# Kernel tuning notes

Measured on AMD Instinct MI355X. Metric: run time of the kernel, lower is better.

The kernel has to match this reference:

```python
import jax, jax.numpy as jnp
import numpy as np

N = 100000   # nodes
E = 1600000  # edges
IN = 128
HID = 64
HEADS = 2
OUT = 16
G = 100      # graphs in batch
NEG_SLOPE = 0.2


def setup_inputs() -> dict:
    key = jax.random.key(0)
    ks = jax.random.split(key, 14)
    s = 0.05
    return {
        "x": jax.random.normal(ks[0], (N, IN), jnp.float32),
        "edge_index": jax.random.randint(ks[1], (2, E), 0, N, dtype=jnp.int32),
        "batch": jnp.sort(jax.random.randint(ks[2], (N,), 0, G, dtype=jnp.int32)),
        "W1": jax.random.normal(ks[3], (IN, HEADS * HID), jnp.float32) * s,
        "att_src1": jax.random.normal(ks[4], (HEADS, HID), jnp.float32) * s,
        "att_dst1": jax.random.normal(ks[5], (HEADS, HID), jnp.float32) * s,
        "b1": jax.random.normal(ks[6], (HEADS * HID,), jnp.float32) * s,
        "W2": jax.random.normal(ks[7], (HEADS * HID, HID), jnp.float32) * s,
        "att_src2": jax.random.normal(ks[8], (1, HID), jnp.float32) * s,
        "att_dst2": jax.random.normal(ks[9], (1, HID), jnp.float32) * s,
        "b2": jax.random.normal(ks[10], (HID,), jnp.float32) * s,
        "Wl": jax.random.normal(ks[11], (HID, OUT), jnp.float32) * s,
        "bl": jax.random.normal(ks[12], (OUT,), jnp.float32) * s,
    }


def gat_conv(x, src, dst, W, a_src, a_dst, b, heads, out_c):
    """PyG GATConv: transform, per-edge attention, segment softmax over dst, scatter-add."""
    n = x.shape[0]
    h = (x @ W).reshape(n, heads, out_c)              # [N, H, C]
    alpha_src = (h * a_src).sum(-1)                   # [N, H]
    alpha_dst = (h * a_dst).sum(-1)                   # [N, H]
    e = jax.nn.leaky_relu(alpha_src[src] + alpha_dst[dst], NEG_SLOPE)  # [Etot, H]
    m = jax.ops.segment_max(e, dst, num_segments=n)   # stable softmax per dst
    ex = jnp.exp(e - m[dst])
    den = jax.ops.segment_sum(ex, dst, num_segments=n)
    alpha = ex / den[dst]                             # [Etot, H]
    msg = h[src] * alpha[..., None]                   # [Etot, H, C]
    out = jax.ops.segment_sum(msg, dst, num_segments=n)
    return out.reshape(n, heads * out_c) + b


def reference(x, edge_index, batch, W1, att_src1, att_dst1, b1,
              W2, att_src2, att_dst2, b2, Wl, bl):
    n = x.shape[0]
    loop = jnp.arange(n, dtype=edge_index.dtype)      # PyG add_self_loops default
    src = jnp.concatenate([edge_index[0], loop])
    dst = jnp.concatenate([edge_index[1], loop])
    h = gat_conv(x, src, dst, W1, att_src1, att_dst1, b1, HEADS, HID)
    h = jax.nn.relu(h)
    h = gat_conv(h, src, dst, W2, att_src2, att_dst2, b2, 1, HID)
    sums = jax.ops.segment_sum(h, batch, num_segments=G)
    cnt = jax.ops.segment_sum(jnp.ones((n,), h.dtype), batch, num_segments=G)
    pooled = sums / jnp.maximum(cnt, 1.0)[:, None]    # global_mean_pool
    return pooled @ Wl + bl
```

## Files before the change

kernel.cpp:

```cpp
#include <hip/hip_runtime.h>
#include <math.h>

#define GRAPHS 100
#define HIDC 64
#define OUTC 16
#define SLOPE 0.2f
#define BSHIFT 8
#define MAXNB 512
#define BKT_CAP 10240

typedef unsigned short ushort_t;
typedef short bf16x8 __attribute__((ext_vector_type(8)));
typedef float f32x4 __attribute__((ext_vector_type(4)));
typedef ushort_t u16x8 __attribute__((ext_vector_type(8)));
typedef ushort_t u16x4 __attribute__((ext_vector_type(4)));

__device__ __forceinline__ float lrelu(float v) { return v > 0.f ? v : SLOPE * v; }
__device__ __forceinline__ void atomAddG(float* p, float v) { unsafeAtomicAdd(p, v); }
__device__ __forceinline__ float bf2f(ushort_t u) {
    unsigned int x = ((unsigned int)u) << 16;
    return __builtin_bit_cast(float, x);
}
__device__ __forceinline__ ushort_t f2bf(float f) {
    unsigned int u = __builtin_bit_cast(unsigned int, f);
    u += 0x7FFFu + ((u >> 16) & 1u);
    return (ushort_t)(u >> 16);
}
__device__ __forceinline__ unsigned int pack2(float lo, float hi) {
    return (unsigned int)f2bf(lo) | ((unsigned int)f2bf(hi) << 16);
}

template <bool A_IS_BF16, int ASTRIDE>
__global__ __launch_bounds__(256) void mfma_gemm_alpha(const void* __restrict__ Av,
                                                       const float* __restrict__ W,
                                                       ushort_t* __restrict__ Cbf,
                                                       const float* __restrict__ att_src,
                                                       const float* __restrict__ att_dst,
                                                       float* __restrict__ asrc,
                                                       float* __restrict__ adst,
                                                       int M, int K, int N) {
    __shared__ ushort_t As[64 * 40];
    __shared__ ushort_t Bs[64 * 40];
    __shared__ float ps[2][64], pd[2][64];
    const int tid = threadIdx.x;
    const int row0 = blockIdx.x * 64;
    const int col0 = blockIdx.y * 64;
    const int lane = tid & 63;
    const int wv = tid >> 6;
    const int wr = (wv >> 1) * 32, wc = (wv & 1) * 32;
    const int l15 = lane & 15, l4 = lane >> 4;

    const int srow = tid >> 2;
    const int skoff = (tid & 3) * 8;
    const int bc = tid & 63, bk = (tid >> 6) * 8;

    f32x4 acc[2][2] = {};

    for (int k0 = 0; k0 < K; k0 += 32) {
        {
            int gr = row0 + srow;
            uint4 v = {0u, 0u, 0u, 0u};
            if (gr < M) {
                if (A_IS_BF16) {
                    const ushort_t* Ab = (const ushort_t*)Av;
                    v = *(const uint4*)(Ab + (size_t)gr * K + k0 + skoff);
                } else {
                    const float* Af = (const float*)Av;
                    const float4 a0 = *(const float4*)(Af + (size_t)gr * K + k0 + skoff);
                    const float4 a1 = *(const float4*)(Af + (size_t)gr * K + k0 + skoff + 4);
                    v.x = pack2(a0.x, a0.y);
                    v.y = pack2(a0.z, a0.w);
                    v.z = pack2(a1.x, a1.y);
                    v.w = pack2(a1.z, a1.w);
                }
            }
            *(uint4*)&As[srow * 40 + skoff] = v;
        }
        {
#pragma unroll
            for (int j = 0; j < 8; ++j) {
                float w = W[(size_t)(k0 + bk + j) * N + col0 + bc];
                Bs[bc * 40 + bk + j] = f2bf(w);
            }
        }
        __syncthreads();
        bf16x8 af[2], bfr[2];
#pragma unroll
        for (int mi = 0; mi < 2; ++mi)
            af[mi] = *(const bf16x8*)&As[(wr + mi * 16 + l15) * 40 + l4 * 8];
#pragma unroll
        for (int ni = 0; ni < 2; ++ni)
            bfr[ni] = *(const bf16x8*)&Bs[(wc + ni * 16 + l15) * 40 + l4 * 8];
#pragma unroll
        for (int mi = 0; mi < 2; ++mi)
#pragma unroll
            for (int ni = 0; ni < 2; ++ni)
                acc[mi][ni] = __builtin_amdgcn_mfma_f32_16x16x32_bf16(af[mi], bfr[ni],
                                                                     acc[mi][ni], 0, 0, 0);
        __syncthreads();
    }
#pragma unroll
    for (int mi = 0; mi < 2; ++mi)
#pragma unroll
        for (int ni = 0; ni < 2; ++ni)
#pragma unroll
            for (int r = 0; r < 4; ++r) {
                int row = row0 + wr + mi * 16 + l4 * 4 + r;
                int colg = col0 + wc + ni * 16 + l15;
                if (row < M) Cbf[(size_t)row * N + colg] = f2bf(acc[mi][ni][r]);
            }
    float as_c[2], ad_c[2];
#pragma unroll
    for (int ni = 0; ni < 2; ++ni) {
        int cidx = col0 + wc + ni * 16 + l15;
        as_c[ni] = att_src[cidx];
        ad_c[ni] = att_dst[cidx];
    }
#pragma unroll
    for (int mi = 0; mi < 2; ++mi)
#pragma unroll
        for (int r = 0; r < 4; ++r) {
            float s = acc[mi][0][r] * as_c[0] + acc[mi][1][r] * as_c[1];
            float d = acc[mi][0][r] * ad_c[0] + acc[mi][1][r] * ad_c[1];
#pragma unroll
            for (int off = 1; off < 16; off <<= 1) {
                s += __shfl_xor(s, off);
                d += __shfl_xor(d, off);
            }
            if (l15 == 0) {
                int rl = wr + mi * 16 + l4 * 4 + r;
                ps[wc >> 5][rl] = s;
                pd[wc >> 5][rl] = d;
            }
        }
    __syncthreads();
    if (tid < 64) {
        int row = row0 + tid;
        if (row < M) {
            asrc[ASTRIDE * row + blockIdx.y] = ps[0][tid] + ps[1][tid];
            adst[ASTRIDE * row + blockIdx.y] = pd[0][tid] + pd[1][tid];
        }
    }
}

__global__ __launch_bounds__(256) void bucket_hist(const int* __restrict__ ei, int E,
                                                   int* __restrict__ bcnt, int NB) {
    __shared__ int h[MAXNB];
    for (int t = threadIdx.x; t < NB; t += 256) h[t] = 0;
    __syncthreads();
    int chunk = (E + gridDim.x - 1) / gridDim.x;
    int e0 = blockIdx.x * chunk;
    int e1 = e0 + chunk < E ? e0 + chunk : E;
    for (int e = e0 + threadIdx.x; e < e1; e += 256)
        atomicAdd(&h[ei[E + e] >> BSHIFT], 1);
    __syncthreads();
    for (int t = threadIdx.x; t < NB; t += 256)
        if (h[t]) atomicAdd(&bcnt[t], h[t]);
}

__global__ __launch_bounds__(512) void bucket_scan(const int* __restrict__ bcnt,
                                                   int* __restrict__ bbase,
                                                   int* __restrict__ bcursor,
                                                   int* __restrict__ rowptr,
                                                   int NB, int n, int E) {
    __shared__ int sh[512];
    int t = threadIdx.x;
    int v = (t < NB) ? bcnt[t] : 0;
    sh[t] = v;
    __syncthreads();
#pragma unroll
    for (int off = 1; off < 512; off <<= 1) {
        int val = (t >= off) ? sh[t - off] : 0;
        __syncthreads();
        sh[t] += val;
        __syncthreads();
    }
    if (t < NB) {
        int base = sh[t] - v;
        bbase[t] = base;
        bcursor[t] = base;
    }
    if (t == 0) {
        bbase[NB] = E;
        rowptr[n] = E;
    }
}

__global__ __launch_bounds__(256) void bucket_scatter(const int* __restrict__ ei, int E,
                                                      int* __restrict__ bcursor,
                                                      unsigned int* __restrict__ ebuf, int NB) {
    __shared__ int h[MAXNB];
    __shared__ int lbase[MAXNB];
    for (int t = threadIdx.x; t < NB; t += 256) h[t] = 0;
    __syncthreads();
    int chunk = (E + gridDim.x - 1) / gridDim.x;
    int e0 = blockIdx.x * chunk;
    int e1 = e0 + chunk < E ? e0 + chunk : E;
    for (int e = e0 + threadIdx.x; e < e1; e += 256)
        atomicAdd(&h[ei[E + e] >> BSHIFT], 1);
    __syncthreads();
    for (int t = threadIdx.x; t < NB; t += 256) {
        int c = h[t];
        lbase[t] = c ? atomicAdd(&bcursor[t], c) : 0;
        h[t] = 0;
    }
    __syncthreads();
    for (int e = e0 + threadIdx.x; e < e1; e += 256) {
        int d = ei[E + e];
        int s = ei[e];
        int b = d >> BSHIFT;
        int off = atomicAdd(&h[b], 1);
        ebuf[lbase[b] + off] = (unsigned)s | ((unsigned)(d & ((1 << BSHIFT) - 1)) << 24);
    }
}

__global__ __launch_bounds__(256) void bucket_build(const unsigned int* __restrict__ ebuf,
                                                    const int* __restrict__ bbase,
                                                    int* __restrict__ rowptr,
                                                    int* __restrict__ col, int n) {
    __shared__ int hist[256];
    __shared__ int curs[256];
    __shared__ int sh[256];
    __shared__ int lsrc[BKT_CAP];
    int b = blockIdx.x;
    int e0 = bbase[b], e1 = bbase[b + 1];
    int cnt = e1 - e0;
    int t = threadIdx.x;
    hist[t] = 0;
    __syncthreads();
    for (int k = t; k < cnt; k += 256) atomicAdd(&hist[ebuf[e0 + k] >> 24], 1);
    __syncthreads();
    int v = hist[t];
    sh[t] = v;
    __syncthreads();
#pragma unroll
    for (int off = 1; off < 256; off <<= 1) {
        int val = (t >= off) ? sh[t - off] : 0;
        __syncthreads();
        sh[t] += val;
        __syncthreads();
    }
    int ex = sh[t] - v;
    curs[t] = ex;
    int node = (b << BSHIFT) + t;
    if (node < n) rowptr[node] = e0 + ex;
    __syncthreads();
    for (int k = t; k < cnt; k += 256) {
        unsigned pk = ebuf[e0 + k];
        int ld = pk >> 24;
        int off = atomicAdd(&curs[ld], 1);
        if (off < BKT_CAP) lsrc[off] = (int)(pk & 0xFFFFFFu);
    }
    __syncthreads();
    int lim = cnt < BKT_CAP ? cnt : BKT_CAP;
    for (int k = t; k < lim; k += 256) col[e0 + k] = lsrc[k];
}

__global__ __launch_bounds__(256) void gat_agg1(const int* __restrict__ rowptr,
                                                const int* __restrict__ col,
                                                const ushort_t* __restrict__ h,
                                                const float* __restrict__ asrc,
                                                const float* __restrict__ adst,
                                                const float* __restrict__ b1,
                                                ushort_t* __restrict__ outb, int n) {
    int i = (blockIdx.x * blockDim.x + threadIdx.x) >> 6;
    if (i >= n) return;
    int lane = threadIdx.x & 63;
    int grp = lane >> 4, c = lane & 15;
    int head = c >> 3;
    float ad = adst[2 * i + head];
    const u16x8* h8 = (const u16x8*)h;
    float acc[8] = {};
    float den = 0.f;
    if (grp == 0) {
        float w = __expf(lrelu(asrc[2 * i + head] + ad));
        u16x8 hv = h8[(size_t)i * 16 + c];
#pragma unroll
        for (int j = 0; j < 8; ++j) acc[j] = bf2f(hv[j]) * w;
        den = w;
    }
    int e0 = rowptr[i], end = rowptr[i + 1];
    for (int e = e0; e < end; e += 16) {
        float wv[4];
        u16x8 hv[4];
#pragma unroll
        for (int q = 0; q < 4; ++q) {
            int idx = e + 4 * q + grp;
            bool vld = idx < end;
            int s = col[vld ? idx : e0];
            float as = asrc[2 * s + head];
            hv[q] = h8[(size_t)s * 16 + c];
            wv[q] = vld ? __expf(lrelu(as + ad)) : 0.f;
        }
#pragma unroll
        for (int q = 0; q < 4; ++q) {
#pragma unroll
            for (int j = 0; j < 8; ++j) acc[j] = fmaf(bf2f(hv[q][j]), wv[q], acc[j]);
            den += wv[q];
        }
    }
#pragma unroll
    for (int j = 0; j < 8; ++j) {
        acc[j] += __shfl_xor(acc[j], 16);
        acc[j] += __shfl_xor(acc[j], 32);
    }
    den += __shfl_xor(den, 16);
    den += __shfl_xor(den, 32);
    if (grp == 0) {
        float inv = 1.f / den;
        u16x8 ov;
#pragma unroll
        for (int j = 0; j < 8; ++j) {
            float r = fmaf(acc[j], inv, b1[8 * c + j]);
            r = r > 0.f ? r : 0.f;
            ov[j] = f2bf(r);
        }
        *((u16x8*)outb + (size_t)i * 16 + c) = ov;
    }
}

__global__ __launch_bounds__(256) void gat_agg2(const int* __restrict__ rowptr,
                                                const int* __restrict__ col,
                                                const ushort_t* __restrict__ h,
                                                const float* __restrict__ asrc,
                                                const float* __restrict__ adst,
                                                ushort_t* __restrict__ outb, int n) {
    int i = (blockIdx.x * blockDim.x + threadIdx.x) >> 6;
    if (i >= n) return;
    int lane = threadIdx.x & 63;
    int grp = lane >> 4, c = lane & 15;
    float ad = adst[i];
    const u16x4* h4 = (const u16x4*)h;
    float acc[4] = {};
    float den = 0.f;
    if (grp == 0) {
        float w = __expf(lrelu(asrc[i] + ad));
        u16x4 hv = h4[(size_t)i * 16 + c];
#pragma unroll
        for (int j = 0; j < 4; ++j) acc[j] = bf2f(hv[j]) * w;
        den = w;
    }
    int e0 = rowptr[i], end = rowptr[i + 1];
    for (int e = e0; e < end; e += 16) {
        float wv[4];
        u16x4 hv[4];
#pragma unroll
        for (int q = 0; q < 4; ++q) {
            int idx = e + 4 * q + grp;
            bool vld = idx < end;
            int s = col[vld ? idx : e0];
            float as = asrc[s];
            hv[q] = h4[(size_t)s * 16 + c];
            wv[q] = vld ? __expf(lrelu(as + ad)) : 0.f;
        }
#pragma unroll
        for (int q = 0; q < 4; ++q) {
#pragma unroll
            for (int j = 0; j < 4; ++j) acc[j] = fmaf(bf2f(hv[q][j]), wv[q], acc[j]);
            den += wv[q];
        }
    }
#pragma unroll
    for (int j = 0; j < 4; ++j) {
        acc[j] += __shfl_xor(acc[j], 16);
        acc[j] += __shfl_xor(acc[j], 32);
    }
    den += __shfl_xor(den, 16);
    den += __shfl_xor(den, 32);
    if (grp == 0) {
        float inv = 1.f / den;
        u16x4 ov = {f2bf(acc[0] * inv), f2bf(acc[1] * inv), f2bf(acc[2] * inv),
                    f2bf(acc[3] * inv)};
        *((u16x4*)outb + (size_t)i * 16 + c) = ov;
    }
}

#define NPB 256
__global__ __launch_bounds__(256) void pool_kernel(const ushort_t* __restrict__ h,
                                                   const int* __restrict__ batch,
                                                   float* __restrict__ sums,
                                                   float* __restrict__ cnt, int n) {
    __shared__ float ls[GRAPHS * HIDC];
    __shared__ float lc[GRAPHS];
    int base = blockIdx.x * NPB;
    for (int t = threadIdx.x; t < GRAPHS * HIDC; t += blockDim.x) ls[t] = 0.f;
    for (int t = threadIdx.x; t < GRAPHS; t += blockDim.x) lc[t] = 0.f;
    __syncthreads();
    int wave = threadIdx.x >> 6, lane = threadIdx.x & 63;
    int end = base + NPB < n ? base + NPB : n;
    for (int i = base + wave; i < end; i += 4) {
        int g = batch[i];
        unsafeAtomicAdd(&ls[g * HIDC + lane], bf2f(h[(size_t)i * HIDC + lane]));
        if (lane == 0) unsafeAtomicAdd(&lc[g], 1.f);
    }
    __syncthreads();
    int gmin = batch[base];
    int gmax = batch[end - 1];
    int ng = gmax - gmin + 1;
    for (int t = threadIdx.x; t < ng * HIDC; t += blockDim.x) {
        int g = gmin + t / HIDC, c = t % HIDC;
        atomAddG(&sums[g * HIDC + c], ls[g * HIDC + c]);
    }
    for (int g = gmin + (int)threadIdx.x; g <= gmax; g += blockDim.x)
        atomAddG(&cnt[g], lc[g]);
}

__global__ void final_kernel(const float* __restrict__ sums, const float* __restrict__ cnt,
                             const float* __restrict__ b2, const float* __restrict__ Wl,
                             const float* __restrict__ bl, float* __restrict__ out) {
    int t = blockIdx.x * blockDim.x + threadIdx.x;
    if (t < GRAPHS * OUTC) {
        int g = t / OUTC, o = t % OUTC;
        float c = cnt[g];
        c = c > 1.f ? c : 1.f;
        float inv = 1.f / c;
        float acc = bl[o];
        for (int k = 0; k < HIDC; ++k)
            acc += (sums[g * HIDC + k] * inv + b2[k]) * Wl[k * OUTC + o];
        out[t] = acc;
    }
}

extern "C" void kernel_launch(void* const* d_in, const int* in_sizes, int n_in, void* d_out,
                              int out_size, void* d_ws, size_t ws_size, hipStream_t stream) {
    const float* x = (const float*)d_in[0];
    const int* ei = (const int*)d_in[1];
    const int* batch = (const int*)d_in[2];
    const float* W1 = (const float*)d_in[3];
    const float* att_src1 = (const float*)d_in[4];
    const float* att_dst1 = (const float*)d_in[5];
    const float* b1 = (const float*)d_in[6];
    const float* W2 = (const float*)d_in[7];
    const float* att_src2 = (const float*)d_in[8];
    const float* att_dst2 = (const float*)d_in[9];
    const float* b2 = (const float*)d_in[10];
    const float* Wl = (const float*)d_in[11];
    const float* bl = (const float*)d_in[12];
    float* out = (float*)d_out;

    const int n = in_sizes[2];
    const int E = in_sizes[1] / 2;

    char* p = (char*)d_ws;
    auto alloc = [&](size_t bytes) {
        char* r = p;
        p += (bytes + 255) & ~(size_t)255;
        return r;
    };
    ushort_t* h1 = (ushort_t*)alloc((size_t)n * 128 * 2);
    ushort_t* hrelu = (ushort_t*)alloc((size_t)n * 128 * 2);
    ushort_t* h2 = (ushort_t*)alloc((size_t)n * 64 * 2);
    ushort_t* conv2 = (ushort_t*)alloc((size_t)n * 64 * 2);
    float* asrc1 = (float*)alloc((size_t)n * 2 * 4);
    float* adst1 = (float*)alloc((size_t)n * 2 * 4);
    float* asrc2 = (float*)alloc((size_t)n * 4);
    float* adst2 = (float*)alloc((size_t)n * 4);
    float* sums = (float*)alloc(GRAPHS * HIDC * 4);
    float* cnt = (float*)alloc(GRAPHS * 4);
    int* bcnt = (int*)alloc(MAXNB * 4);
    int* bbase = (int*)alloc((MAXNB + 1) * 4);
    int* bcursor = (int*)alloc(MAXNB * 4);
    int* rowptr = (int*)alloc(((size_t)n + 1) * 4);
    unsigned int* ebuf = (unsigned int*)alloc((size_t)E * 4);
    int* col = (int*)alloc((size_t)E * 4);

    const int NB = (n + 255) >> BSHIFT;
    const int gblk = (n + 63) / 64;

    hipMemsetAsync(bcnt, 0, NB * sizeof(int), stream);
    bucket_hist<<<512, 256, 0, stream>>>(ei, E, bcnt, NB);
    bucket_scan<<<1, 512, 0, stream>>>(bcnt, bbase, bcursor, rowptr, NB, n, E);
    bucket_scatter<<<512, 256, 0, stream>>>(ei, E, bcursor, ebuf, NB);
    bucket_build<<<NB, 256, 0, stream>>>(ebuf, bbase, rowptr, col, n);

    mfma_gemm_alpha<false, 2><<<dim3(gblk, 2), 256, 0, stream>>>(
        x, W1, h1, att_src1, att_dst1, asrc1, adst1, n, 128, 128);
    gat_agg1<<<(n + 3) / 4, 256, 0, stream>>>(rowptr, col, h1, asrc1, adst1, b1, hrelu, n);

    mfma_gemm_alpha<true, 1><<<dim3(gblk, 1), 256, 0, stream>>>(
        hrelu, W2, h2, att_src2, att_dst2, asrc2, adst2, n, 128, 64);
    gat_agg2<<<(n + 3) / 4, 256, 0, stream>>>(rowptr, col, h2, asrc2, adst2, conv2, n);

    hipMemsetAsync(sums, 0, (GRAPHS * HIDC + GRAPHS) * sizeof(float), stream);
    pool_kernel<<<(n + NPB - 1) / NPB, 256, 0, stream>>>(conv2, batch, sums, cnt, n);
    final_kernel<<<(GRAPHS * OUTC + 255) / 256, 256, 0, stream>>>(sums, cnt, b2, Wl, bl, out);
}
```

Baseline: 363.2 us.

## Fuse edge scatter with layer-1 GEMM and pack bf16 FMAs in aggregation

Merges the bucket scatter kernel and the first-layer GEMM+attention kernel into one launch, with blocks split by index, so the two independent stages run concurrently and one launch is saved. The zeroing of the pooling buffers moves into the scan kernel, which removes a memset. The aggregation kernels now decode bf16 pairs straight from 32-bit words and use 2-wide vector FMAs (packed-math candidates), with 32-bit byte-offset addressing in place of 64-bit index math. The fused kernel's shared-memory footprint is the union of both stages, which may lower occupancy, and the unsigned offsets assume node offsets stay under 4 GB.

```diff
diff --git a/kernel.cpp b/kernel.cpp
--- a/kernel.cpp
+++ b/kernel.cpp
@@ -8,10 +8,12 @@
 #define BSHIFT 8
 #define MAXNB 512
 #define BKT_CAP 10240
+#define SCAT_BLOCKS 512
 
 typedef unsigned short ushort_t;
 typedef short bf16x8 __attribute__((ext_vector_type(8)));
 typedef float f32x4 __attribute__((ext_vector_type(4)));
+typedef float f32x2 __attribute__((ext_vector_type(2)));
 typedef ushort_t u16x8 __attribute__((ext_vector_type(8)));
 typedef ushort_t u16x4 __attribute__((ext_vector_type(4)));
 
@@ -29,27 +31,26 @@
 __device__ __forceinline__ unsigned int pack2(float lo, float hi) {
     return (unsigned int)f2bf(lo) | ((unsigned int)f2bf(hi) << 16);
 }
+__device__ __forceinline__ void mac2(unsigned int u, float w, f32x2& a) {
+    f32x2 hv;
+    hv.x = __builtin_bit_cast(float, u << 16);
+    hv.y = __builtin_bit_cast(float, u & 0xFFFF0000u);
+    f32x2 w2 = {w, w};
+    a = __builtin_elementwise_fma(hv, w2, a);
+}
 
 template <bool A_IS_BF16, int ASTRIDE>
-__global__ __launch_bounds__(256) void mfma_gemm_alpha(const void* __restrict__ Av,
-                                                       const float* __restrict__ W,
-                                                       ushort_t* __restrict__ Cbf,
-                                                       const float* __restrict__ att_src,
-                                                       const float* __restrict__ att_dst,
-                                                       float* __restrict__ asrc,
-                                                       float* __restrict__ adst,
-                                                       int M, int K, int N) {
-    __shared__ ushort_t As[64 * 40];
-    __shared__ ushort_t Bs[64 * 40];
-    __shared__ float ps[2][64], pd[2][64];
+__device__ __forceinline__ void gemm_alpha_body(
+    const void* __restrict__ Av, const float* __restrict__ W, ushort_t* __restrict__ Cbf,
+    const float* __restrict__ att_src, const float* __restrict__ att_dst,
+    float* __restrict__ asrc, float* __restrict__ adst, int M, int K, int N,
+    int row0, int head, ushort_t* As, ushort_t* Bs, float (*ps)[64], float (*pd)[64]) {
     const int tid = threadIdx.x;
-    const int row0 = blockIdx.x * 64;
-    const int col0 = blockIdx.y * 64;
+    const int col0 = head * 64;
     const int lane = tid & 63;
     const int wv = tid >> 6;
     const int wr = (wv >> 1) * 32, wc = (wv & 1) * 32;
     const int l15 = lane & 15, l4 = lane >> 4;
-
     const int srow = tid >> 2;
     const int skoff = (tid & 3) * 8;
     const int bc = tid & 63, bk = (tid >> 6) * 8;
@@ -137,10 +138,26 @@
     if (tid < 64) {
         int row = row0 + tid;
         if (row < M) {
-            asrc[ASTRIDE * row + blockIdx.y] = ps[0][tid] + ps[1][tid];
-            adst[ASTRIDE * row + blockIdx.y] = pd[0][tid] + pd[1][tid];
-        }
-    }
+            asrc[ASTRIDE * row + head] = ps[0][tid] + ps[1][tid];
+            adst[ASTRIDE * row + head] = pd[0][tid] + pd[1][tid];
+        }
+    }
+}
+
+template <bool A_IS_BF16, int ASTRIDE>
+__global__ __launch_bounds__(256) void mfma_gemm_alpha(const void* __restrict__ Av,
+                                                       const float* __restrict__ W,
+                                                       ushort_t* __restrict__ Cbf,
+                                                       const float* __restrict__ att_src,
+                                                       const float* __restrict__ att_dst,
+                                                       float* __restrict__ asrc,
+                                                       float* __restrict__ adst,
+                                                       int M, int K, int N) {
+    __shared__ ushort_t As[64 * 40];
+    __shared__ ushort_t Bs[64 * 40];
+    __shared__ float ps[2][64], pd[2][64];
+    gemm_alpha_body<A_IS_BF16, ASTRIDE>(Av, W, Cbf, att_src, att_dst, asrc, adst, M, K, N,
+                                        blockIdx.x * 64, blockIdx.y, As, Bs, ps, pd);
 }
 
 __global__ __launch_bounds__(256) void bucket_hist(const int* __restrict__ ei, int E,
@@ -162,6 +179,8 @@
                                                    int* __restrict__ bbase,
                                                    int* __restrict__ bcursor,
                                                    int* __restrict__ rowptr,
+                                                   float* __restrict__ sums,
+                                                   float* __restrict__ cnt,
                                                    int NB, int n, int E) {
     __shared__ int sh[512];
     int t = threadIdx.x;
@@ -184,33 +203,49 @@
         bbase[NB] = E;
         rowptr[n] = E;
     }
-}
-
-__global__ __launch_bounds__(256) void bucket_scatter(const int* __restrict__ ei, int E,
-                                                      int* __restrict__ bcursor,
-                                                      unsigned int* __restrict__ ebuf, int NB) {
-    __shared__ int h[MAXNB];
+    for (int k = t; k < GRAPHS * HIDC; k += 512) sums[k] = 0.f;
+    for (int k = t; k < GRAPHS; k += 512) cnt[k] = 0.f;
+}
+
+__global__ __launch_bounds__(256) void scatter_gemm1(
+    const int* __restrict__ ei, int E, int* __restrict__ bcursor,
+    unsigned int* __restrict__ ebuf, int NB,
+    const float* __restrict__ x, const float* __restrict__ W, ushort_t* __restrict__ h1,
+    const float* __restrict__ att_src, const float* __restrict__ att_dst,
+    float* __restrict__ asrc, float* __restrict__ adst, int M, int gblk) {
+    __shared__ ushort_t As[64 * 40];
+    __shared__ ushort_t Bs[64 * 40];
+    __shared__ float ps[2][64], pd[2][64];
+    __shared__ int hh[MAXNB];
     __shared__ int lbase[MAXNB];
-    for (int t = threadIdx.x; t < NB; t += 256) h[t] = 0;
-    __syncthreads();
-    int chunk = (E + gridDim.x - 1) / gridDim.x;
-    int e0 = blockIdx.x * chunk;
-    int e1 = e0 + chunk < E ? e0 + chunk : E;
-    for (int e = e0 + threadIdx.x; e < e1; e += 256)
-        atomicAdd(&h[ei[E + e] >> BSHIFT], 1);
-    __syncthreads();
-    for (int t = threadIdx.x; t < NB; t += 256) {
-        int c = h[t];
-        lbase[t] = c ? atomicAdd(&bcursor[t], c) : 0;
-        h[t] = 0;
-    }
-    __syncthreads();
-    for (int e = e0 + threadIdx.x; e < e1; e += 256) {
-        int d = ei[E + e];
-        int s = ei[e];
-        int b = d >> BSHIFT;
-        int off = atomicAdd(&h[b], 1);
-        ebuf[lbase[b] + off] = (unsigned)s | ((unsigned)(d & ((1 << BSHIFT) - 1)) << 24);
+    if ((int)blockIdx.x < SCAT_BLOCKS) {
+        for (int t = threadIdx.x; t < NB; t += 256) hh[t] = 0;
+        __syncthreads();
+        int chunk = (E + SCAT_BLOCKS - 1) / SCAT_BLOCKS;
+        int e0 = blockIdx.x * chunk;
+        int e1 = e0 + chunk < E ? e0 + chunk : E;
+        for (int e = e0 + threadIdx.x; e < e1; e += 256)
+            atomicAdd(&hh[ei[E + e] >> BSHIFT], 1);
+        __syncthreads();
+        for (int t = threadIdx.x; t < NB; t += 256) {
+            int c = hh[t];
+            lbase[t] = c ? atomicAdd(&bcursor[t], c) : 0;
+            hh[t] = 0;
+        }
+        __syncthreads();
+        for (int e = e0 + threadIdx.x; e < e1; e += 256) {
+            int d = ei[E + e];
+            int s = ei[e];
+            int b = d >> BSHIFT;
+            int off = atomicAdd(&hh[b], 1);
+            ebuf[lbase[b] + off] = (unsigned)s | ((unsigned)(d & ((1 << BSHIFT) - 1)) << 24);
+        }
+    } else {
+        int bid = blockIdx.x - SCAT_BLOCKS;
+        int head = bid / gblk;
+        int row0 = (bid - head * gblk) * 64;
+        gemm_alpha_body<false, 2>(x, W, h1, att_src, att_dst, asrc, adst, M, 128, 128,
+                                  row0, head, As, Bs, ps, pd);
     }
 }
 
@@ -268,41 +303,50 @@
     int lane = threadIdx.x & 63;
     int grp = lane >> 4, c = lane & 15;
     int head = c >> 3;
+    const char* hb = (const char*)h;
+    const char* ab = (const char*)asrc;
     float ad = adst[2 * i + head];
-    const u16x8* h8 = (const u16x8*)h;
-    float acc[8] = {};
+    f32x2 acc2[4] = {};
     float den = 0.f;
+    unsigned coff = (unsigned)c << 4;
     if (grp == 0) {
         float w = __expf(lrelu(asrc[2 * i + head] + ad));
-        u16x8 hv = h8[(size_t)i * 16 + c];
-#pragma unroll
-        for (int j = 0; j < 8; ++j) acc[j] = bf2f(hv[j]) * w;
+        uint4 hq = *(const uint4*)(hb + (((unsigned)i << 8) + coff));
+        mac2(hq.x, w, acc2[0]);
+        mac2(hq.y, w, acc2[1]);
+        mac2(hq.z, w, acc2[2]);
+        mac2(hq.w, w, acc2[3]);
         den = w;
     }
     int e0 = rowptr[i], end = rowptr[i + 1];
+    unsigned aoff = ((unsigned)head << 2);
     for (int e = e0; e < end; e += 16) {
         float wv[4];
-        u16x8 hv[4];
+        uint4 hq[4];
 #pragma unroll
         for (int q = 0; q < 4; ++q) {
             int idx = e + 4 * q + grp;
             bool vld = idx < end;
             int s = col[vld ? idx : e0];
-            float as = asrc[2 * s + head];
-            hv[q] = h8[(size_t)s * 16 + c];
+            float as = *(const float*)(ab + (((unsigned)s << 3) + aoff));
+            hq[q] = *(const uint4*)(hb + (((unsigned)s << 8) + coff));
             wv[q] = vld ? __expf(lrelu(as + ad)) : 0.f;
         }
 #pragma unroll
         for (int q = 0; q < 4; ++q) {
-#pragma unroll
-            for (int j = 0; j < 8; ++j) acc[j] = fmaf(bf2f(hv[q][j]), wv[q], acc[j]);
+            mac2(hq[q].x, wv[q], acc2[0]);
+            mac2(hq[q].y, wv[q], acc2[1]);
+            mac2(hq[q].z, wv[q], acc2[2]);
+            mac2(hq[q].w, wv[q], acc2[3]);
             den += wv[q];
         }
     }
 #pragma unroll
-    for (int j = 0; j < 8; ++j) {
-        acc[j] += __shfl_xor(acc[j], 16);
-        acc[j] += __shfl_xor(acc[j], 32);
+    for (int k = 0; k < 4; ++k) {
+        acc2[k].x += __shfl_xor(acc2[k].x, 16);
+        acc2[k].x += __shfl_xor(acc2[k].x, 32);
+        acc2[k].y += __shfl_xor(acc2[k].y, 16);
+        acc2[k].y += __shfl_xor(acc2[k].y, 32);
     }
     den += __shfl_xor(den, 16);
     den += __shfl_xor(den, 32);
@@ -310,10 +354,13 @@
         float inv = 1.f / den;
         u16x8 ov;
 #pragma unroll
-        for (int j = 0; j < 8; ++j) {
-            float r = fmaf(acc[j], inv, b1[8 * c + j]);
-            r = r > 0.f ? r : 0.f;
-            ov[j] = f2bf(r);
+        for (int k = 0; k < 4; ++k) {
+            float r0 = fmaf(acc2[k].x, inv, b1[8 * c + 2 * k]);
+            float r1 = fmaf(acc2[k].y, inv, b1[8 * c + 2 * k + 1]);
+            r0 = r0 > 0.f ? r0 : 0.f;
+            r1 = r1 > 0.f ? r1 : 0.f;
+            ov[2 * k] = f2bf(r0);
+            ov[2 * k + 1] = f2bf(r1);
         }
         *((u16x8*)outb + (size_t)i * 16 + c) = ov;
     }
@@ -329,48 +376,52 @@
     if (i >= n) return;
     int lane = threadIdx.x & 63;
     int grp = lane >> 4, c = lane & 15;
+    const char* hb = (const char*)h;
+    const char* ab = (const char*)asrc;
     float ad = adst[i];
-    const u16x4* h4 = (const u16x4*)h;
-    float acc[4] = {};
+    f32x2 acc2[2] = {};
     float den = 0.f;
+    unsigned coff = (unsigned)c << 3;
     if (grp == 0) {
         float w = __expf(lrelu(asrc[i] + ad));
-        u16x4 hv = h4[(size_t)i * 16 + c];
-#pragma unroll
-        for (int j = 0; j < 4; ++j) acc[j] = bf2f(hv[j]) * w;
+        uint2 hq = *(const uint2*)(hb + (((unsigned)i << 7) + coff));
+        mac2(hq.x, w, acc2[0]);
+        mac2(hq.y, w, acc2[1]);
         den = w;
     }
     int e0 = rowptr[i], end = rowptr[i + 1];
     for (int e = e0; e < end; e += 16) {
         float wv[4];
-        u16x4 hv[4];
+        uint2 hq[4];
 #pragma unroll
         for (int q = 0; q < 4; ++q) {
             int idx = e + 4 * q + grp;
             bool vld = idx < end;
             int s = col[vld ? idx : e0];
-            float as = asrc[s];
-            hv[q] = h4[(size_t)s * 16 + c];
+            float as = *(const float*)(ab + ((unsigned)s << 2));
+            hq[q] = *(const uint2*)(hb + (((unsigned)s << 7) + coff));
             wv[q] = vld ? __expf(lrelu(as + ad)) : 0.f;
         }
 #pragma unroll
         for (int q = 0; q < 4; ++q) {
-#pragma unroll
-            for (int j = 0; j < 4; ++j) acc[j] = fmaf(bf2f(hv[q][j]), wv[q], acc[j]);
+            mac2(hq[q].x, wv[q], acc2[0]);
+            mac2(hq[q].y, wv[q], acc2[1]);
             den += wv[q];
         }
     }
 #pragma unroll
-    for (int j = 0; j < 4; ++j) {
-        acc[j] += __shfl_xor(acc[j], 16);
-        acc[j] += __shfl_xor(acc[j], 32);
+    for (int k = 0; k < 2; ++k) {
+        acc2[k].x += __shfl_xor(acc2[k].x, 16);
+        acc2[k].x += __shfl_xor(acc2[k].x, 32);
+        acc2[k].y += __shfl_xor(acc2[k].y, 16);
+        acc2[k].y += __shfl_xor(acc2[k].y, 32);
     }
     den += __shfl_xor(den, 16);
     den += __shfl_xor(den, 32);
     if (grp == 0) {
         float inv = 1.f / den;
-        u16x4 ov = {f2bf(acc[0] * inv), f2bf(acc[1] * inv), f2bf(acc[2] * inv),
-                    f2bf(acc[3] * inv)};
+        u16x4 ov = {f2bf(acc2[0].x * inv), f2bf(acc2[0].y * inv), f2bf(acc2[1].x * inv),
+                    f2bf(acc2[1].y * inv)};
         *((u16x4*)outb + (size_t)i * 16 + c) = ov;
     }
 }
@@ -468,20 +519,18 @@
     const int gblk = (n + 63) / 64;
 
     hipMemsetAsync(bcnt, 0, NB * sizeof(int), stream);
-    bucket_hist<<<512, 256, 0, stream>>>(ei, E, bcnt, NB);
-    bucket_scan<<<1, 512, 0, stream>>>(bcnt, bbase, bcursor, rowptr, NB, n, E);
-    bucket_scatter<<<512, 256, 0, stream>>>(ei, E, bcursor, ebuf, NB);
+    bucket_hist<<<SCAT_BLOCKS, 256, 0, stream>>>(ei, E, bcnt, NB);
+    bucket_scan<<<1, 512, 0, stream>>>(bcnt, bbase, bcursor, rowptr, sums, cnt, NB, n, E);
+    scatter_gemm1<<<SCAT_BLOCKS + 2 * gblk, 256, 0, stream>>>(
+        ei, E, bcursor, ebuf, NB, x, W1, h1, att_src1, att_dst1, asrc1, adst1, n, gblk);
     bucket_build<<<NB, 256, 0, stream>>>(ebuf, bbase, rowptr, col, n);
 
-    mfma_gemm_alpha<false, 2><<<dim3(gblk, 2), 256, 0, stream>>>(
-        x, W1, h1, att_src1, att_dst1, asrc1, adst1, n, 128, 128);
     gat_agg1<<<(n + 3) / 4, 256, 0, stream>>>(rowptr, col, h1, asrc1, adst1, b1, hrelu, n);
 
     mfma_gemm_alpha<true, 1><<<dim3(gblk, 1), 256, 0, stream>>>(
         hrelu, W2, h2, att_src2, att_dst2, asrc2, adst2, n, 128, 64);
     gat_agg2<<<(n + 3) / 4, 256, 0, stream>>>(rowptr, col, h2, asrc2, adst2, conv2, n);
 
-    hipMemsetAsync(sums, 0, (GRAPHS * HIDC + GRAPHS) * sizeof(float), stream);
     pool_kernel<<<(n + NPB - 1) / NPB, 256, 0, stream>>>(conv2, batch, sums, cnt, n);
     final_kernel<<<(GRAPHS * OUTC + 255) / 256, 256, 0, stream>>>(sums, cnt, b2, Wl, bl, out);
 }
```

Result: no change. 366.7 us (+1.0%).
